# Kernel optimization log

Measured on AMD Instinct MI355X. Metric: run time of the kernel, lower is better.

Reference implementation:

```python
import jax, jax.numpy as jnp
import numpy as np

B, P, T, R, A = 16384, 3, 2, 3, 3   # batch, n_players, teammates, rivals, action_dim
HID = [1024, 512]
ENC_OUT = 64
RIVAL_START = 9 * 9 + 12 * P       # 117, as in the torch module
NEG_SLOPE = 0.01                    # nn.LeakyReLU default


def _linpack(key, k, din, dout):
    # PyTorch nn.Linear default init: U(-1/sqrt(din), 1/sqrt(din))
    kw, kb = jax.random.split(key)
    bound = 1.0 / np.sqrt(din)
    W = jax.random.uniform(kw, (k, din, dout), jnp.float32, -bound, bound)
    b = jax.random.uniform(kb, (k, dout), jnp.float32, -bound, bound)
    return W, b


def setup_inputs() -> dict:
    key = jax.random.key(0)
    ks = jax.random.split(key, 16)
    obs = jax.random.normal(ks[0], (B, P, 144), jnp.float32)
    act = jax.random.normal(ks[1], (B, P, A), jnp.float32)
    # stacked per-segment encoder weights (grouped small GEMMs)
    Wp1, bp1 = _linpack(ks[2], 9, 2 + A, 32)
    Wp2, bp2 = _linpack(ks[3], 9, 32, ENC_OUT)
    Wt1, bt1 = _linpack(ks[4], T, 12, 32)
    Wt2, bt2 = _linpack(ks[5], T, 32, ENC_OUT)
    Wr1, br1 = _linpack(ks[6], R, 9, 32)
    Wr2, br2 = _linpack(ks[7], R, 32, ENC_OUT)
    # q head: [P*896] -> 1024 -> 512 -> P
    din = P * (9 + T + R) * ENC_OUT
    Wq1, bq1 = _linpack(ks[8], 1, din, HID[0]);  Wq1, bq1 = Wq1[0], bq1[0]
    Wq2, bq2 = _linpack(ks[9], 1, HID[0], HID[1]); Wq2, bq2 = Wq2[0], bq2[0]
    Wq3, bq3 = _linpack(ks[10], 1, HID[1], P);   Wq3, bq3 = Wq3[0], bq3[0]
    return dict(obs=obs, act=act,
                Wp1=Wp1, bp1=bp1, Wp2=Wp2, bp2=bp2,
                Wt1=Wt1, bt1=bt1, Wt2=Wt2, bt2=bt2,
                Wr1=Wr1, br1=br1, Wr2=Wr2, br2=br2,
                Wq1=Wq1, bq1=bq1, Wq2=Wq2, bq2=bq2, Wq3=Wq3, bq3=bq3)


def _enc2(x, W1, b1, W2, b2):
    # x: [B, P, K, din]; W1: [K, din, 32]; W2: [K, 32, 64] -> [B, P, K, 64]
    lrelu = lambda v: jax.nn.leaky_relu(v, NEG_SLOPE)
    h = lrelu(jnp.einsum('bpki,kio->bpko', x, W1) + b1)
    return lrelu(jnp.einsum('bpkh,kho->bpko', h, W2) + b2)


def reference(obs, act, Wp1, bp1, Wp2, bp2, Wt1, bt1, Wt2, bt2,
              Wr1, br1, Wr2, br2, Wq1, bq1, Wq2, bq2, Wq3, bq3):
    b = obs.shape[0]
    # prop segments: obs[:, :, 2i:2i+2] concat act  -> [B, P, 9, 2+A]
    x_prop = jnp.concatenate(
        [obs[:, :, :18].reshape(b, P, 9, 2),
         jnp.broadcast_to(act[:, :, None, :], (b, P, 9, A))], axis=-1)
    x_team = obs[:, :, 18:18 + 12 * T].reshape(b, P, T, 12)
    x_riv = obs[:, :, RIVAL_START:RIVAL_START + 9 * R].reshape(b, P, R, 9)
    ep = _enc2(x_prop, Wp1, bp1, Wp2, bp2)   # [B, P, 9, 64]
    et = _enc2(x_team, Wt1, bt1, Wt2, bt2)   # [B, P, T, 64]
    er = _enc2(x_riv, Wr1, br1, Wr2, br2)    # [B, P, R, 64]
    enc = jnp.concatenate([ep, et, er], axis=2).reshape(b, -1)  # [B, P*14*64]
    # q head: ReLU hidden activations, identity output
    h = jax.nn.relu(enc @ Wq1 + bq1)
    h = jax.nn.relu(h @ Wq2 + bq2)
    return h @ Wq3 + bq3                      # [B, P]
```

## Files before the change

kernel.cpp:

```cpp
#include <hip/hip_runtime.h>
#include <hip/hip_bf16.h>
#include <cstdint>

typedef __bf16 bf16x8 __attribute__((ext_vector_type(8)));
typedef float f32x4 __attribute__((ext_vector_type(4)));

__device__ __forceinline__ void gld16(const __bf16* g, __bf16* lds) {
    __builtin_amdgcn_global_load_lds(
        (__attribute__((address_space(1))) void*)(uintptr_t)g,
        (__attribute__((address_space(3))) void*)(uint32_t)(uintptr_t)lds,
        16, 0, 0);
}

__global__ __launch_bounds__(256) void prep_all(const float* __restrict__ Wq1, const float* __restrict__ Wq2,
                                                const float* __restrict__ Wp1, const float* __restrict__ bp1,
                                                const float* __restrict__ Wp2, const float* __restrict__ bp2,
                                                const float* __restrict__ Wt1, const float* __restrict__ bt1,
                                                const float* __restrict__ Wt2, const float* __restrict__ bt2,
                                                const float* __restrict__ Wr1, const float* __restrict__ br1,
                                                const float* __restrict__ Wr2, const float* __restrict__ br2,
                                                __bf16* __restrict__ w1t, __bf16* __restrict__ w2t,
                                                float* __restrict__ w1p, __bf16* __restrict__ w2e) {
    __shared__ float t[64][65];
    const int idx = blockIdx.x, tid = threadIdx.x;
    if (idx < 800) {
        const float* in; __bf16* out; int R, C, bx, by;
        if (idx < 672) { in = Wq1; out = w1t; R = 2688; C = 1024; bx = idx % 42; by = idx / 42; }
        else { const int i2 = idx - 672; in = Wq2; out = w2t; R = 1024; C = 512; bx = i2 % 16; by = i2 / 16; }
        const int r0 = bx * 64, c0 = by * 64;
#pragma unroll
        for (int i = 0; i < 16; i++) {
            int id2 = i * 256 + tid;
            int rr = id2 >> 6, cc = id2 & 63;
            t[rr][cc] = in[(size_t)(r0 + rr) * C + (c0 + cc)];
        }
        __syncthreads();
#pragma unroll
        for (int i = 0; i < 16; i++) {
            int id2 = i * 256 + tid;
            int rr = id2 >> 6, cc = id2 & 63;
            out[(size_t)(c0 + rr) * R + (r0 + cc)] = (__bf16)t[cc][rr];
        }
    } else {
        const int s = idx - 800;
        int ks, din, w1off;
        const float *W1, *B1, *W2, *B2;
        if (s < 9)      { ks = s;      din = 5;  w1off = s * 160;
                          W1 = Wp1; B1 = bp1; W2 = Wp2; B2 = bp2; }
        else if (s < 11){ ks = s - 9;  din = 12; w1off = 1440 + ks * 384;
                          W1 = Wt1; B1 = bt1; W2 = Wt2; B2 = bt2; }
        else            { ks = s - 11; din = 9;  w1off = 2208 + ks * 288;
                          W1 = Wr1; B1 = br1; W2 = Wr2; B2 = br2; }
        W1 += ks * din * 32; B1 += ks * 32; W2 += ks * 2048; B2 += ks * 64;
        for (int i = tid; i < din * 32; i += 256) w1p[w1off + i] = W1[i];
        if (tid < 32) w1p[3072 + s * 32 + tid] = B1[tid];
        if (tid < 64) w1p[3520 + s * 64 + tid] = B2[tid];
        for (int i = tid; i < 2048; i += 256) {
            const int o = i >> 5, k = i & 31;
            w2e[s * 2048 + i] = (__bf16)W2[k * 64 + o];
        }
    }
}

__global__ __launch_bounds__(256) void enc_fused(const float* __restrict__ obs,
                                                 const float* __restrict__ act,
                                                 const float* __restrict__ w1p,
                                                 const __bf16* __restrict__ w2t,
                                                 __bf16* __restrict__ enc) {
    __shared__ float sW[4416];
    __shared__ __bf16 sH[2][64 * 40];
    __shared__ __align__(16) __bf16 sO[2][64 * 72];
    const int tid = threadIdx.x;
    for (int i = tid; i < 4416; i += 256) sW[i] = w1p[i];
    const int rloc = tid >> 2, q = tid & 3;
    const int row = blockIdx.x * 64 + rloc;
    const float* orow = obs + (size_t)row * 144;
    const float a0 = act[row * 3], a1 = act[row * 3 + 1], a2 = act[row * 3 + 2];
    const int wv = tid >> 6, lane = tid & 63;
    const int fr = lane & 15, kq = lane >> 4;

    bf16x8 bfrA[4], bfrB[4];
    int curH = 0, curO = 0;

    auto prefetchB = [&](int sn) {
#pragma unroll
        for (int n = 0; n < 4; n++)
            bfrB[n] = *(const bf16x8*)&w2t[(sn * 64 + n * 16 + fr) * 32 + kq * 8];
    };
    auto storeOut = [&](int sp, int bO) {
#pragma unroll
        for (int h = 0; h < 2; h++) {
            const int c = tid + h * 256;
            const int r = c >> 3, ch = c & 7;
            const bf16x8 v = *(const bf16x8*)&sO[bO][r * 72 + ch * 8];
            *(bf16x8*)&enc[((size_t)blockIdx.x * 64 + r) * 896 + sp * 64 + ch * 8] = v;
        }
    };
    auto l2c = [&](int s, int bH, int bO) {
        const bf16x8 afr = *(const bf16x8*)&sH[bH][(wv * 16 + fr) * 40 + kq * 8];
        f32x4 acc[4] = {};
#pragma unroll
        for (int n = 0; n < 4; n++)
            acc[n] = __builtin_amdgcn_mfma_f32_16x16x32_bf16(afr, bfrA[n], acc[n], 0, 0, 0);
        const float* b2 = sW + 3520 + s * 64;
#pragma unroll
        for (int n = 0; n < 4; n++) {
            const float bv = b2[n * 16 + fr];
#pragma unroll
            for (int rg = 0; rg < 4; rg++) {
                float v = acc[n][rg] + bv;
                v = fmaxf(v, 0.01f * v);
                sO[bO][(wv * 16 + kq * 4 + rg) * 72 + n * 16 + fr] = (__bf16)v;
            }
        }
    };

#define L1(DIN, W1OFF, SGI, DH, XLOAD)                               \
    {                                                                \
        float x[DIN];                                                \
        XLOAD;                                                       \
        const float* w1 = sW + (W1OFF);                              \
        const float* b1 = sW + 3072 + (SGI) * 32;                    \
        bf16x8 t_;                                                   \
        _Pragma("unroll") for (int j = 0; j < 8; j++) {              \
            const int o = q * 8 + j;                                 \
            float a_ = b1[o];                                        \
            _Pragma("unroll") for (int i = 0; i < DIN; i++)          \
                a_ += x[i] * w1[i * 32 + o];                         \
            t_[j] = (__bf16)fmaxf(a_, 0.01f * a_);                   \
        }                                                            \
        *(bf16x8*)&sH[DH][rloc * 40 + q * 8] = t_;                   \
    }

#define PROPX(K) { x[0] = orow[2 * (K)]; x[1] = orow[2 * (K) + 1]; x[2] = a0; x[3] = a1; x[4] = a2; }
#define TEAMX(K) { _Pragma("unroll") for (int i = 0; i < 12; i++) x[i] = orow[18 + 12 * (K) + i]; }
#define RIVX(K)  { _Pragma("unroll") for (int i = 0; i < 9; i++) x[i] = orow[117 + 9 * (K) + i]; }

#define STEP(S, NEXTL1)                                              \
    __syncthreads();                                                 \
    if ((S) < 13) prefetchB((S) + 1);                                \
    if ((S) > 0) storeOut((S) - 1, curO ^ 1);                        \
    l2c((S), curH, curO);                                            \
    _Pragma("unroll") for (int n = 0; n < 4; n++) bfrA[n] = bfrB[n]; \
    NEXTL1                                                           \
    curH ^= 1; curO ^= 1;

    prefetchB(0);
    __syncthreads();
#pragma unroll
    for (int n = 0; n < 4; n++) bfrA[n] = bfrB[n];
    L1(5, 0, 0, 0, PROPX(0))

    STEP(0,  L1(5, 160, 1, curH ^ 1, PROPX(1)))
    STEP(1,  L1(5, 320, 2, curH ^ 1, PROPX(2)))
    STEP(2,  L1(5, 480, 3, curH ^ 1, PROPX(3)))
    STEP(3,  L1(5, 640, 4, curH ^ 1, PROPX(4)))
    STEP(4,  L1(5, 800, 5, curH ^ 1, PROPX(5)))
    STEP(5,  L1(5, 960, 6, curH ^ 1, PROPX(6)))
    STEP(6,  L1(5, 1120, 7, curH ^ 1, PROPX(7)))
    STEP(7,  L1(5, 1280, 8, curH ^ 1, PROPX(8)))
    STEP(8,  L1(12, 1440, 9, curH ^ 1, TEAMX(0)))
    STEP(9,  L1(12, 1824, 10, curH ^ 1, TEAMX(1)))
    STEP(10, L1(9, 2208, 11, curH ^ 1, RIVX(0)))
    STEP(11, L1(9, 2496, 12, curH ^ 1, RIVX(1)))
    STEP(12, L1(9, 2784, 13, curH ^ 1, RIVX(2)))
    STEP(13, )

    __syncthreads();
    storeOut(13, curO ^ 1);
#undef STEP
#undef L1
#undef PROPX
#undef TEAMX
#undef RIVX
}

template <int NB, bool HEAD, int SCHED>
__global__ __launch_bounds__(512, 2) void gemm256_relu(const __bf16* __restrict__ Ag,
                                                       const __bf16* __restrict__ Btg,
                                                       const float* __restrict__ bias,
                                                       __bf16* __restrict__ Cg,
                                                       const float* __restrict__ Wq3,
                                                       float* __restrict__ pout,
                                                       int N, int K, int lgn) {
    __shared__ __align__(16) __bf16 ldsF[32768 + 2 * 2 * NB * 4096];
    const int tid = threadIdx.x;
    const int wid = tid >> 6, lane = tid & 63;
    const int wm = wid >> 2, wn = wid & 3;
    const int fr = lane & 15, kq = lane >> 4;

    const int chunk = gridDim.x >> 3;
    const int wg = (blockIdx.x & 7) * chunk + (blockIdx.x >> 3);
    const int bn = wg & ((1 << lgn) - 1), bm = wg >> lgn;

    const int c0 = tid, c1 = tid + 512;
    const int r0 = c0 >> 3, s0 = (c0 & 7) ^ (r0 & 7);
    const int r1 = c1 >> 3, s1 = (c1 & 7) ^ (r1 & 7);
    const size_t aH = (size_t)128 * K;
    const size_t bH = (size_t)(NB * 64) * K;
    const __bf16* aB0 = Ag + (size_t)(bm * 256 + r0) * K + s0 * 8;
    const __bf16* aB1 = Ag + (size_t)(bm * 256 + r1) * K + s1 * 8;
    const __bf16* bB0 = Btg + (size_t)(bn * (NB * 128) + r0) * K + s0 * 8;
    const __bf16* bB1 = Btg + (size_t)(bn * (NB * 128) + r1) * K + s1 * 8;

    f32x4 acc[2][2][4][NB] = {};
    bf16x8 a0[4][2], a1[4][2], b0[NB][2], b1[NB][2];

#define LDSA(BUF, H) (ldsF + ((BUF) * 2 + (H)) * 8192)
#define LDSB(BUF, H) (ldsF + 32768 + ((BUF) * 2 + (H)) * (NB * 4096))

#define STAGE_A(BUF, H, KO)                                   \
    do {                                                      \
        __bf16* d_ = LDSA(BUF, H);                            \
        gld16(aB0 + (H)*aH + (KO), d_ + c0 * 8);              \
        gld16(aB1 + (H)*aH + (KO), d_ + c1 * 8);              \
    } while (0)
#define STAGE_B(BUF, H, KO)                                   \
    do {                                                      \
        __bf16* d_ = LDSB(BUF, H);                            \
        gld16(bB0 + (H)*bH + (KO), d_ + c0 * 8);              \
        if constexpr (NB == 2) gld16(bB1 + (H)*bH + (KO), d_ + c1 * 8); \
    } while (0)

#define LDFA(BUF, H, ROW, KS) \
    (*(const bf16x8*)&LDSA(BUF, H)[(ROW) * 64 + ((((KS)*4 + kq) ^ ((ROW)&7)) * 8)])
#define LDFB(BUF, H, ROW, KS) \
    (*(const bf16x8*)&LDSB(BUF, H)[(ROW) * 64 + ((((KS)*4 + kq) ^ ((ROW)&7)) * 8)])

#define LOAD_A(BUF, H, DST)                                   \
    _Pragma("unroll") for (int m = 0; m < 4; m++)             \
        _Pragma("unroll") for (int ks = 0; ks < 2; ks++)      \
            DST[m][ks] = LDFA(BUF, H, wm * 64 + m * 16 + fr, ks);
#define LOAD_B(BUF, H, DST)                                   \
    _Pragma("unroll") for (int n = 0; n < NB; n++)            \
        _Pragma("unroll") for (int ks = 0; ks < 2; ks++)      \
            DST[n][ks] = LDFB(BUF, H, wn * (NB * 16) + n * 16 + fr, ks);

#define MM(Q, R, AR, BR)                                      \
    __builtin_amdgcn_s_setprio(1);                            \
    _Pragma("unroll") for (int ks = 0; ks < 2; ks++)          \
        _Pragma("unroll") for (int m = 0; m < 4; m++)         \
            _Pragma("unroll") for (int n = 0; n < NB; n++)    \
                acc[Q][R][m][n] = __builtin_amdgcn_mfma_f32_16x16x32_bf16( \
                    AR[m][ks], BR[n][ks], acc[Q][R][m][n], 0, 0, 0); \
    __builtin_amdgcn_s_setprio(0);

#define SB0 __builtin_amdgcn_sched_barrier(0)
#define BAR __builtin_amdgcn_s_barrier()
#define LGKM(NSTR) asm volatile("s_waitcnt lgkmcnt(" NSTR ")" ::: "memory")
#define LGKM2(N2, N1)                                         \
    if constexpr (NB == 2) LGKM(#N2); else LGKM(#N1);
#define VMW(NSTR) asm volatile("s_waitcnt vmcnt(" NSTR ")" ::: "memory")
#define VMW2(N2, N1)                                          \
    if constexpr (NB == 2) VMW(#N2); else VMW(#N1);

    const int NT = K >> 6;

    if constexpr (SCHED == 0) {
        STAGE_A(0, 0, 0);
        STAGE_B(0, 0, 0);
        STAGE_B(0, 1, 0);
        STAGE_A(0, 1, 0);
        VMW("2");
        BAR;
        LOAD_A(0, 0, a0)
        LOAD_B(0, 0, b0)
        SB0;

        for (int t = 0; t < NT - 1; ++t) {
            const int buf = t & 1, nb = buf ^ 1;
            const int kO = (t + 1) << 6;

            STAGE_A(nb, 0, kO);
            STAGE_B(nb, 0, kO);
            VMW2(4, 3);
            LOAD_B(buf, 1, b1)
            SB0;
            BAR;
            LGKM2(4, 2);
            SB0;
            MM(0, 0, a0, b0)

            STAGE_B(nb, 1, kO);
            STAGE_A(nb, 1, kO);
            LOAD_A(buf, 1, a1)
            SB0;
            BAR;
            LGKM("8");
            SB0;
            MM(0, 1, a0, b1)

            BAR;
            LGKM("0");
            SB0;
            MM(1, 0, a1, b0)

            VMW("2");
            BAR;
            LOAD_A(nb, 0, a0)
            LOAD_B(nb, 0, b0)
            SB0;
            MM(1, 1, a1, b1)
        }

        {
            const int buf = (NT - 1) & 1;
            VMW("0");
            LOAD_B(buf, 1, b1)
            SB0;
            BAR;
            LGKM2(4, 2);
            SB0;
            MM(0, 0, a0, b0)

            LOAD_A(buf, 1, a1)
            SB0;
            BAR;
            LGKM("8");
            SB0;
            MM(0, 1, a0, b1)

            BAR;
            LGKM("0");
            SB0;
            MM(1, 0, a1, b0)

            MM(1, 1, a1, b1)
        }
    } else {
        STAGE_A(0, 0, 0);
        STAGE_B(0, 0, 0);
        STAGE_B(0, 1, 0);
        STAGE_A(0, 1, 0);

        for (int t = 0; t < NT; ++t) {
            const int buf = t & 1, nb = buf ^ 1;
            const int kO = (t + 1) << 6;

            VMW("0");
            BAR;
            LOAD_A(buf, 0, a0)
            LOAD_B(buf, 0, b0)
            SB0;
            if (t + 1 < NT) {
                STAGE_A(nb, 0, kO);
                STAGE_B(nb, 0, kO);
                STAGE_B(nb, 1, kO);
                STAGE_A(nb, 1, kO);
            }
            SB0;
            LOAD_B(buf, 1, b1)
            LOAD_A(buf, 1, a1)
            SB0;
            LGKM2(12, 10);
            SB0;
            MM(0, 0, a0, b0)
            LGKM("8");
            SB0;
            MM(0, 1, a0, b1)
            LGKM("0");
            SB0;
            MM(1, 0, a1, b0)
            MM(1, 1, a1, b1)
        }
    }

    const int cc = lane & 15, rr = (lane >> 4) << 2;
    if constexpr (!HEAD) {
#pragma unroll
        for (int q = 0; q < 2; q++)
#pragma unroll
            for (int r2 = 0; r2 < 2; r2++)
#pragma unroll
                for (int m = 0; m < 4; m++)
#pragma unroll
                    for (int n = 0; n < NB; n++) {
                        const int colG = bn * (NB * 128) + r2 * (NB * 64) + wn * (NB * 16) + n * 16 + cc;
                        const int rowG = bm * 256 + q * 128 + wm * 64 + m * 16 + rr;
                        const float bv = bias[colG];
#pragma unroll
                        for (int reg = 0; reg < 4; reg++) {
                            float v = acc[q][r2][m][n][reg] + bv;
                            v = fmaxf(v, 0.0f);
                            Cg[(size_t)(rowG + reg) * N + colG] = (__bf16)v;
                        }
                    }
    } else {
        __syncthreads();
        __bf16* hS = ldsF;
#pragma unroll
        for (int q = 0; q < 2; q++)
#pragma unroll
            for (int r2 = 0; r2 < 2; r2++)
#pragma unroll
                for (int m = 0; m < 4; m++) {
                    const int colL = r2 * 64 + wn * 16 + cc;
                    const int rowL0 = q * 128 + wm * 64 + m * 16 + rr;
                    const float bv = bias[bn * 128 + colL];
                    const int slot = colL >> 3, pos = colL & 7;
#pragma unroll
                    for (int reg = 0; reg < 4; reg++) {
                        const int rowL = rowL0 + reg;
                        float v = acc[q][r2][m][0][reg] + bv;
                        v = fmaxf(v, 0.0f);
                        hS[rowL * 128 + (slot ^ (rowL & 7)) * 8 + pos] = (__bf16)v;
                    }
                }
        __syncthreads();
        const int rowL = tid >> 1, half = tid & 1;
        float s0v = 0.f, s1v = 0.f, s2v = 0.f;
#pragma unroll
        for (int c8 = 0; c8 < 8; c8++) {
            const int lslot = half * 8 + c8;
            const int pslot = half * 8 + (c8 ^ (rowL & 7));
            const bf16x8 hv = *(const bf16x8*)&hS[rowL * 128 + pslot * 8];
#pragma unroll
            for (int j = 0; j < 8; j++) {
                const float hf = (float)hv[j];
                const int col = bn * 128 + lslot * 8 + j;
                s0v += hf * Wq3[col * 3 + 0];
                s1v += hf * Wq3[col * 3 + 1];
                s2v += hf * Wq3[col * 3 + 2];
            }
        }
        s0v += __shfl_xor(s0v, 1);
        s1v += __shfl_xor(s1v, 1);
        s2v += __shfl_xor(s2v, 1);
        if (!half) {
            float* p = pout + ((size_t)(bm * 256 + rowL) * 4 + bn) * 3;
            p[0] = s0v; p[1] = s1v; p[2] = s2v;
        }
    }
#undef LDSA
#undef LDSB
#undef STAGE_A
#undef STAGE_B
#undef LDFA
#undef LDFB
#undef LOAD_A
#undef LOAD_B
#undef MM
#undef SB0
#undef BAR
#undef LGKM
#undef LGKM2
#undef VMW
#undef VMW2
}

__global__ __launch_bounds__(256) void reduce_head(const float* __restrict__ pout,
                                                   const float* __restrict__ bq3,
                                                   float* __restrict__ out) {
    const int row = blockIdx.x * 256 + threadIdx.x;
    const float* p = pout + (size_t)row * 12;
#pragma unroll
    for (int j = 0; j < 3; j++)
        out[(size_t)row * 3 + j] = p[j] + p[3 + j] + p[6 + j] + p[9 + j] + bq3[j];
}

extern "C" void kernel_launch(void* const* d_in, const int* in_sizes, int n_in,
                              void* d_out, int out_size, void* d_ws, size_t ws_size,
                              hipStream_t stream) {
    const float* obs = (const float*)d_in[0];
    const float* act = (const float*)d_in[1];
    const float* Wp1 = (const float*)d_in[2];  const float* bp1 = (const float*)d_in[3];
    const float* Wp2 = (const float*)d_in[4];  const float* bp2 = (const float*)d_in[5];
    const float* Wt1 = (const float*)d_in[6];  const float* bt1 = (const float*)d_in[7];
    const float* Wt2 = (const float*)d_in[8];  const float* bt2 = (const float*)d_in[9];
    const float* Wr1 = (const float*)d_in[10]; const float* br1 = (const float*)d_in[11];
    const float* Wr2 = (const float*)d_in[12]; const float* br2 = (const float*)d_in[13];
    const float* Wq1 = (const float*)d_in[14]; const float* bq1 = (const float*)d_in[15];
    const float* Wq2 = (const float*)d_in[16]; const float* bq2 = (const float*)d_in[17];
    const float* Wq3 = (const float*)d_in[18]; const float* bq3 = (const float*)d_in[19];
    float* out = (float*)d_out;

    char* ws = (char*)d_ws;
    __bf16* enc  = (__bf16*)(ws);
    __bf16* h1   = (__bf16*)(ws + 88080384);
    float*  pout = (float*)(ws + 88080384 + 33554432);
    __bf16* w1t  = (__bf16*)(ws + 138412032);
    __bf16* w2t  = (__bf16*)(ws + 143917056);
    float*  w1p  = (float*)(ws + 144965632);
    __bf16* w2e  = (__bf16*)(ws + 144983296);

    prep_all<<<814, 256, 0, stream>>>(Wq1, Wq2, Wp1, bp1, Wp2, bp2, Wt1, bt1, Wt2, bt2,
                                      Wr1, br1, Wr2, br2, w1t, w2t, w1p, w2e);

    enc_fused<<<768, 256, 0, stream>>>(obs, act, w1p, w2e, enc);

    gemm256_relu<2, false, 0><<<dim3(256), 512, 0, stream>>>(enc, w1t, bq1, h1, nullptr, nullptr, 1024, 2688, 2);
    gemm256_relu<1, true, 1><<<dim3(256), 512, 0, stream>>>(h1, w2t, bq2, nullptr, Wq3, pout, 512, 1024, 2);
    reduce_head<<<64, 256, 0, stream>>>(pout, bq3, out);
}
```

Baseline: 136.2 us.

## Add interleaved stage/compute schedule variant for first head GEMM

Adds a third software-pipeline schedule (SCHED==2) to the 256-tile GEMM. It spreads the global-to-LDS staging of the next K tile across the four MFMA sub-blocks, using finer-grained vmcnt and lgkmcnt waits and barriers. The first q-head GEMM is switched to this schedule. The aim is better overlap of memory staging with matrix math, at the cost of more barriers per iteration.

```diff
diff --git a/kernel.cpp b/kernel.cpp
--- a/kernel.cpp
+++ b/kernel.cpp
@@ -302,7 +302,6 @@
             SB0;
             MM(1, 1, a1, b1)
         }
-
         {
             const int buf = (NT - 1) & 1;
             VMW("0");
@@ -327,7 +326,7 @@
 
             MM(1, 1, a1, b1)
         }
-    } else {
+    } else if constexpr (SCHED == 1) {
         STAGE_A(0, 0, 0);
         STAGE_B(0, 0, 0);
         STAGE_B(0, 1, 0);
@@ -362,6 +361,56 @@
             SB0;
             MM(1, 0, a1, b0)
             MM(1, 1, a1, b1)
+        }
+    } else {
+        STAGE_A(0, 0, 0);
+        STAGE_B(0, 0, 0);
+        STAGE_B(0, 1, 0);
+        STAGE_A(0, 1, 0);
+        VMW2(4, 3);
+        BAR;
+
+        for (int t = 0; t < NT; ++t) {
+            const int buf = t & 1, nb = buf ^ 1;
+            const int kO = (t + 1) << 6;
+            const bool st = (t + 1 < NT);
+
+            LOAD_A(buf, 0, a0)
+            LOAD_B(buf, 0, b0)
+            if (st) STAGE_A(nb, 0, kO);
+            LGKM("8");
+            SB0;
+            BAR;
+            LGKM("0");
+            SB0;
+            MM(0, 0, a0, b0)
+            if (st) { VMW("4"); } else { VMW("2"); }
+            BAR;
+
+            LOAD_B(buf, 1, b1)
+            if (st) STAGE_B(nb, 0, kO);
+            SB0;
+            BAR;
+            LGKM("0");
+            SB0;
+            MM(0, 1, a0, b1)
+            if (st) { VMW2(4, 3); } else { VMW("0"); }
+            BAR;
+
+            LOAD_A(buf, 1, a1)
+            if (st) STAGE_B(nb, 1, kO);
+            SB0;
+            BAR;
+            LGKM("0");
+            SB0;
+            MM(1, 0, a1, b0)
+            BAR;
+
+            if (st) STAGE_A(nb, 1, kO);
+            SB0;
+            MM(1, 1, a1, b1)
+            if (st) { VMW2(4, 3); }
+            BAR;
         }
     }
 
@@ -488,7 +537,7 @@
 
     enc_fused<<<768, 256, 0, stream>>>(obs, act, w1p, w2e, enc);
 
-    gemm256_relu<2, false, 0><<<dim3(256), 512, 0, stream>>>(enc, w1t, bq1, h1, nullptr, nullptr, 1024, 2688, 2);
+    gemm256_relu<2, false, 2><<<dim3(256), 512, 0, stream>>>(enc, w1t, bq1, h1, nullptr, nullptr, 1024, 2688, 2);
     gemm256_relu<1, true, 1><<<dim3(256), 512, 0, stream>>>(h1, w2t, bq2, nullptr, Wq3, pout, 512, 1024, 2);
     reduce_head<<<64, 256, 0, stream>>>(pout, bq3, out);
 }
```

Result: slower. 142.2 us, median of 2 (+4.4%).
